# Kernel tuning notes

Hardware: AMD Instinct MI355X
Metric: run time of the kernel (lower is better)

The kernel has to match this reference:

```python
import jax, jax.numpy as jnp
import numpy as np

B = 32768
W = 7            # window_size (fixed: classifier head outputs 7*2 -> view(B, 7, 2))
F = 80           # per-frame feature size
WF = W * F       # window_feature_size = 560
EH = 512         # encoder_hidden_size
EO = 512         # encoder_output_size
H = 512          # core_hidden_size
NUM_STEPS = 7
EPS = 1e-5

def _linear(x, w, b):
    return x @ w.T + b

def _bn(x, g, bt, m, v):
    # BatchNorm1d in eval mode (running stats)
    return (x - m) * g / jnp.sqrt(v + EPS) + bt

def _ln(x, g, b):
    mu = x.mean(-1, keepdims=True)
    var = x.var(-1, keepdims=True)
    return (x - mu) / jnp.sqrt(var + EPS) * g + b

def setup_inputs():
    key = jax.random.key(0)
    ks = iter(jax.random.split(key, 40))
    def rn(shape, s=0.05):
        return jax.random.normal(next(ks), shape, dtype=jnp.float32) * s
    def rv(shape):
        return jax.random.uniform(next(ks), shape, dtype=jnp.float32) + 0.5
    return {
        'features': jax.random.normal(next(ks), (B, W, F), dtype=jnp.float32),
        'dec_w': rn((W, H)), 'dec_b': rn((W,)),
        'dec_bn_g': rv((W,)), 'dec_bn_b': rn((W,)), 'dec_bn_m': rn((W,)), 'dec_bn_v': rv((W,)),
        'ea1_w': rn((EH, W)), 'ea1_b': rn((EH,)),
        'ea1_bn_g': rv((EH,)), 'ea1_bn_b': rn((EH,)), 'ea1_bn_m': rn((EH,)), 'ea1_bn_v': rv((EH,)),
        'ea2_w': rn((EO, EH)), 'ea2_b': rn((EO,)),
        'ea2_bn_g': rv((EO,)), 'ea2_bn_b': rn((EO,)), 'ea2_bn_m': rn((EO,)), 'ea2_bn_v': rv((EO,)),
        'ei1_w': rn((EH, WF)), 'ei1_b': rn((EH,)),
        'ei1_bn_g': rv((EH,)), 'ei1_bn_b': rn((EH,)), 'ei1_bn_m': rn((EH,)), 'ei1_bn_v': rv((EH,)),
        'ei2_w': rn((EO, EH)), 'ei2_b': rn((EO,)),
        'ei2_bn_g': rv((EO,)), 'ei2_bn_b': rn((EO,)), 'ei2_bn_m': rn((EO,)), 'ei2_bn_v': rv((EO,)),
        'w_ih': rn((4 * H, EO)), 'w_hh': rn((4 * H, H)), 'b_ih': rn((4 * H,)), 'b_hh': rn((4 * H,)),
        'ln_g': rv((H,)), 'ln_b': rn((H,)),
        'cls_w': rn((2 * W, H)), 'cls_b': rn((2 * W,)),
    }

def _forward(features, dec_w, dec_b, dec_bn_g, dec_bn_b, dec_bn_m, dec_bn_v,
             ea1_w, ea1_b, ea1_bn_g, ea1_bn_b, ea1_bn_m, ea1_bn_v,
             ea2_w, ea2_b, ea2_bn_g, ea2_bn_b, ea2_bn_m, ea2_bn_v,
             ei1_w, ei1_b, ei1_bn_g, ei1_bn_b, ei1_bn_m, ei1_bn_v,
             ei2_w, ei2_b, ei2_bn_g, ei2_bn_b, ei2_bn_m, ei2_bn_v,
             w_ih, w_hh, b_ih, b_hh, ln_g, ln_b, cls_w, cls_b):
    Bsz = features.shape[0]

    def encoder(att):
        # attention branch: Linear -> BN -> ReLU -> Linear -> BN
        a = jax.nn.relu(_bn(_linear(att, ea1_w, ea1_b), ea1_bn_g, ea1_bn_b, ea1_bn_m, ea1_bn_v))
        a = _bn(_linear(a, ea2_w, ea2_b), ea2_bn_g, ea2_bn_b, ea2_bn_m, ea2_bn_v)
        # attended-input branch on flattened (features * att)
        ai = (features * att[:, :, None]).reshape(Bsz, WF)
        x = jax.nn.relu(_bn(_linear(ai, ei1_w, ei1_b), ei1_bn_g, ei1_bn_b, ei1_bn_m, ei1_bn_v))
        x = _bn(_linear(x, ei2_w, ei2_b), ei2_bn_g, ei2_bn_b, ei2_bn_m, ei2_bn_v)
        return jax.nn.relu(a + x)

    def lstm_step(x, h, c):
        gates = x @ w_ih.T + b_ih + h @ w_hh.T + b_hh  # [B, 4H], torch gate order i,f,g,o
        i, f, g, o = jnp.split(gates, 4, axis=-1)
        c = jax.nn.sigmoid(f) * c + jax.nn.sigmoid(i) * jnp.tanh(g)
        h = jax.nn.sigmoid(o) * jnp.tanh(c)
        return h, c

    # initial pass: uniform attention, zero LSTM state (state=None -> no LN)
    att0 = jnp.full((Bsz, W), 1.0 / W, dtype=features.dtype)
    h, c = lstm_step(encoder(att0), jnp.zeros((Bsz, H), features.dtype), jnp.zeros((Bsz, H), features.dtype))

    def body(carry, _):
        h, c = carry
        # decoder: Linear -> BN -> smooth softmax
        logits = _bn(_linear(h, dec_w, dec_b), dec_bn_g, dec_bn_b, dec_bn_m, dec_bn_v)
        s = jax.nn.sigmoid(logits)
        att = s / s.sum(-1, keepdims=True)
        agg = encoder(att)
        hn, cn = lstm_step(agg, _ln(h, ln_g, ln_b), _ln(c, ln_g, ln_b))
        return (hn, cn), None

    (h, c), _ = jax.lax.scan(body, (h, c), None, length=NUM_STEPS)
    out = _linear(h, cls_w, cls_b).reshape(Bsz, W, 2)
    return jax.nn.log_softmax(out, axis=2)

def reference(features, dec_w, dec_b, dec_bn_g, dec_bn_b, dec_bn_m, dec_bn_v,
              ea1_w, ea1_b, ea1_bn_g, ea1_bn_b, ea1_bn_m, ea1_bn_v,
              ea2_w, ea2_b, ea2_bn_g, ea2_bn_b, ea2_bn_m, ea2_bn_v,
              ei1_w, ei1_b, ei1_bn_g, ei1_bn_b, ei1_bn_m, ei1_bn_v,
              ei2_w, ei2_b, ei2_bn_g, ei2_bn_b, ei2_bn_m, ei2_bn_v,
              w_ih, w_hh, b_ih, b_hh, ln_g, ln_b, cls_w, cls_b):
    return _forward(features, dec_w, dec_b, dec_bn_g, dec_bn_b, dec_bn_m, dec_bn_v,
                    ea1_w, ea1_b, ea1_bn_g, ea1_bn_b, ea1_bn_m, ea1_bn_v,
                    ea2_w, ea2_b, ea2_bn_g, ea2_bn_b, ea2_bn_m, ea2_bn_v,
                    ei1_w, ei1_b, ei1_bn_g, ei1_bn_b, ei1_bn_m, ei1_bn_v,
                    ei2_w, ei2_b, ei2_bn_g, ei2_bn_b, ei2_bn_m, ei2_bn_v,
                    w_ih, w_hh, b_ih, b_hh, ln_g, ln_b, cls_w, cls_b)
```

## Files before the change

### kernel.cpp

```cpp
#include <hip/hip_runtime.h>
#include <cstdint>
#include <cstddef>

#define BSZ 32768
#define WN 7
#define WF 560
#define K1P 576
#define EPS 1e-5f

typedef __attribute__((ext_vector_type(8))) short bf16x8;
typedef __attribute__((ext_vector_type(4))) float f32x4;

__device__ __forceinline__ float b2f(short s) {
  union { float f; unsigned u; } x; x.u = ((unsigned)(unsigned short)s) << 16; return x.f;
}
__device__ __forceinline__ short f2b(float f) {
  union { float f; unsigned u; } x; x.f = f;
  unsigned r = x.u + 0x7fffu + ((x.u >> 16) & 1u);
  return (short)(r >> 16);
}
__device__ __forceinline__ float sigf(float x) { return 1.0f / (1.0f + __expf(-x)); }
__device__ __forceinline__ float ftanh(float x) {
  float t = __expf(-2.0f * fabsf(x));
  float r = (1.0f - t) / (1.0f + t);
  return copysignf(r, x);
}

__device__ __forceinline__ void async_copy16(const short* g, short* l) {
  __builtin_amdgcn_global_load_lds((const __attribute__((address_space(1))) unsigned*)g,
                                   (__attribute__((address_space(3))) unsigned*)l, 16, 0, 0);
}


__global__ void fold_small_k(const float* __restrict__ dec_w, const float* __restrict__ dec_b,
                             const float* __restrict__ dec_g, const float* __restrict__ dec_bt,
                             const float* __restrict__ dec_m, const float* __restrict__ dec_v,
                             const float* __restrict__ ea1_w, const float* __restrict__ ea1_b,
                             const float* __restrict__ ea1_g, const float* __restrict__ ea1_bt,
                             const float* __restrict__ ea1_m, const float* __restrict__ ea1_v,
                             float* __restrict__ decwf, float* __restrict__ decb8,
                             float* __restrict__ ea1f)
{
  int t = blockIdx.x * 256 + threadIdx.x;
  if (t < 7 * 512) {
    int w = t >> 9;
    float s = dec_g[w] * rsqrtf(dec_v[w] + EPS);
    decwf[t] = dec_w[t] * s;
  }
  if (t < 8) {
    if (t < 7) {
      float s = dec_g[t] * rsqrtf(dec_v[t] + EPS);
      decb8[t] = (dec_b[t] - dec_m[t]) * s + dec_bt[t];
    } else decb8[t] = 0.0f;
  }
  if (t < 512) {
    float s = ea1_g[t] * rsqrtf(ea1_v[t] + EPS);
    #pragma unroll
    for (int w = 0; w < 7; ++w) ea1f[t * 8 + w] = ea1_w[t * 7 + w] * s;
    ea1f[t * 8 + 7] = (ea1_b[t] - ea1_m[t]) * s + ea1_bt[t];
  }
}

__global__ void fold_ei1_k(const float* __restrict__ w, const float* __restrict__ b,
                           const float* __restrict__ g, const float* __restrict__ bt,
                           const float* __restrict__ m, const float* __restrict__ v,
                           short* __restrict__ ei1f, float* __restrict__ bias1)
{
  int idx = blockIdx.x * 256 + threadIdx.x;
  int n = idx / K1P, k = idx % K1P;
  float s = g[n] * rsqrtf(v[n] + EPS);
  ei1f[idx] = (k < WF) ? f2b(w[n * WF + k] * s) : (short)0;
  if (k == 0) bias1[n] = (b[n] - m[n]) * s + bt[n];
}

__global__ void fold_w2_k(const float* __restrict__ wi, const float* __restrict__ bi,
                          const float* __restrict__ gi, const float* __restrict__ bti,
                          const float* __restrict__ mi, const float* __restrict__ vi,
                          const float* __restrict__ wa, const float* __restrict__ ba,
                          const float* __restrict__ ga, const float* __restrict__ bta,
                          const float* __restrict__ ma, const float* __restrict__ va,
                          short* __restrict__ W2, float* __restrict__ bias2)
{
  int idx = blockIdx.x * 256 + threadIdx.x;
  int n = idx >> 10, k = idx & 1023;
  float si = gi[n] * rsqrtf(vi[n] + EPS);
  float sa = ga[n] * rsqrtf(va[n] + EPS);
  float val = (k < 512) ? wi[n * 512 + k] * si : wa[n * 512 + (k - 512)] * sa;
  W2[idx] = f2b(val);
  if (k == 0)
    bias2[n] = (bi[n] - mi[n]) * si + bti[n] + (ba[n] - ma[n]) * sa + bta[n];
}

__global__ void fold_wg_k(const float* __restrict__ w_ih, const float* __restrict__ w_hh,
                          const float* __restrict__ b_ih, const float* __restrict__ b_hh,
                          short* __restrict__ Wg, float* __restrict__ biasg)
{
  int idx = blockIdx.x * 256 + threadIdx.x;
  int c = idx >> 10, k = idx & 1023;
  int g = (c >> 4) & 3;
  int u = (c >> 6) * 16 + (c & 15);
  int r = g * 512 + u;
  float val = (k < 512) ? w_ih[r * 512 + k] : w_hh[r * 512 + (k - 512)];
  Wg[idx] = f2b(val);
  if (k == 0) biasg[c] = b_ih[r] + b_hh[r];
}

__global__ __launch_bounds__(512)
void attln_k(const float* __restrict__ hbuf, const float* __restrict__ cbuf,
             const float* __restrict__ decwf, const float* __restrict__ decb8,
             const float* __restrict__ ea1f,
             const float* __restrict__ ln_g, const float* __restrict__ ln_b,
             const float* __restrict__ feat,
             short* __restrict__ ghA, short* __restrict__ c_ln,
             short* __restrict__ xa, short* __restrict__ ai, int init)
{
  const int lane = threadIdx.x & 63;
  const int b = blockIdx.x * 8 + (threadIdx.x >> 6);
  float av[WN];
  if (init) {
    const float c7 = 1.0f / 7.0f;
    #pragma unroll
    for (int w = 0; w < WN; ++w) av[w] = c7;
    int4 z = make_int4(0, 0, 0, 0);
    *(int4*)&ghA[b * 1024 + 512 + lane * 8] = z;
    *(int4*)&c_ln[b * 512 + lane * 8] = z;
  } else {
    float hl[8];
    const float* hp = hbuf + (size_t)b * 512 + lane * 8;
    *(float4*)&hl[0] = *(const float4*)hp;
    *(float4*)&hl[4] = *(const float4*)(hp + 4);
    float s = 0.f, s2 = 0.f;
    #pragma unroll
    for (int e = 0; e < 8; ++e) { s += hl[e]; s2 += hl[e] * hl[e]; }
    float p[WN];
    #pragma unroll
    for (int w = 0; w < WN; ++w) {
      const float* dw = decwf + w * 512 + lane * 8;
      float4 w0 = *(const float4*)dw, w1 = *(const float4*)(dw + 4);
      p[w] = hl[0] * w0.x + hl[1] * w0.y + hl[2] * w0.z + hl[3] * w0.w
           + hl[4] * w1.x + hl[5] * w1.y + hl[6] * w1.z + hl[7] * w1.w;
    }
    #pragma unroll
    for (int o = 32; o > 0; o >>= 1) {
      s  += __shfl_xor(s, o);
      s2 += __shfl_xor(s2, o);
      #pragma unroll
      for (int w = 0; w < WN; ++w) p[w] += __shfl_xor(p[w], o);
    }
    float mu = s * (1.0f / 512.0f);
    float var = s2 * (1.0f / 512.0f) - mu * mu;
    float rstd = rsqrtf(var + EPS);
    float ssum = 0.f;
    #pragma unroll
    for (int w = 0; w < WN; ++w) { float sg = sigf(p[w] + decb8[w]); av[w] = sg; ssum += sg; }
    float inv = 1.0f / ssum;
    #pragma unroll
    for (int w = 0; w < WN; ++w) av[w] *= inv;
    short o8[8];
    #pragma unroll
    for (int e = 0; e < 8; ++e) {
      int i = lane * 8 + e;
      o8[e] = f2b((hl[e] - mu) * rstd * ln_g[i] + ln_b[i]);
    }
    *(int4*)&ghA[b * 1024 + 512 + lane * 8] = *(int4*)o8;
    float cl[8];
    const float* cp = cbuf + (size_t)b * 512 + lane * 8;
    *(float4*)&cl[0] = *(const float4*)cp;
    *(float4*)&cl[4] = *(const float4*)(cp + 4);
    float cs = 0.f, cs2 = 0.f;
    #pragma unroll
    for (int e = 0; e < 8; ++e) { cs += cl[e]; cs2 += cl[e] * cl[e]; }
    #pragma unroll
    for (int o = 32; o > 0; o >>= 1) {
      cs  += __shfl_xor(cs, o);
      cs2 += __shfl_xor(cs2, o);
    }
    float cmu = cs * (1.0f / 512.0f);
    float cvar = cs2 * (1.0f / 512.0f) - cmu * cmu;
    float crstd = rsqrtf(cvar + EPS);
    #pragma unroll
    for (int e = 0; e < 8; ++e) {
      int i = lane * 8 + e;
      o8[e] = f2b((cl[e] - cmu) * crstd * ln_g[i] + ln_b[i]);
    }
    *(int4*)&c_ln[b * 512 + lane * 8] = *(int4*)o8;
  }
  short a8[8];
  #pragma unroll
  for (int e = 0; e < 8; ++e) {
    int n = lane * 8 + e;
    const float* wr = ea1f + n * 8;
    float4 w0 = *(const float4*)wr, w1 = *(const float4*)(wr + 4);
    float v = w1.w
            + av[0] * w0.x + av[1] * w0.y + av[2] * w0.z + av[3] * w0.w
            + av[4] * w1.x + av[5] * w1.y + av[6] * w1.z;
    a8[e] = f2b(fmaxf(v, 0.0f));
  }
  *(int4*)&xa[b * 1024 + 512 + lane * 8] = *(int4*)a8;
  const float* fr = feat + (size_t)b * WF;
  short* air = ai + (size_t)b * K1P;
  #pragma unroll
  for (int rr = 0; rr < 2; ++rr) {
    int c8 = lane + rr * 64;
    if (c8 < 72) {
      int k = c8 * 8;
      short s8[8];
      if (k < WF) {
        int window = c8 / 10;
        float a = av[0];
        #pragma unroll
        for (int w = 1; w < WN; ++w) a = (window == w) ? av[w] : a;
        float4 f0 = *(const float4*)(fr + k);
        float4 f1 = *(const float4*)(fr + k + 4);
        s8[0] = f2b(f0.x * a); s8[1] = f2b(f0.y * a); s8[2] = f2b(f0.z * a); s8[3] = f2b(f0.w * a);
        s8[4] = f2b(f1.x * a); s8[5] = f2b(f1.y * a); s8[6] = f2b(f1.z * a); s8[7] = f2b(f1.w * a);
      } else {
        #pragma unroll
        for (int e = 0; e < 8; ++e) s8[e] = 0;
      }
      *(int4*)&air[k] = *(int4*)s8;
    }
  }
}

#define STAGE128(SRC, LD, K0, S) do {                                          \
    _Pragma("unroll")                                                          \
    for (int r_ = 0; r_ < 4; ++r_) {                                           \
      int idx_ = r_ * 256 + t;                                                 \
      int row_ = idx_ >> 3, dcol_ = (idx_ & 7) * 8;                            \
      int scol_ = dcol_ ^ ((row_ & 7) << 3);                                   \
      async_copy16(SRC + (size_t)row_ * (LD) + (K0) + scol_, &S[idx_ * 8]);    \
    }                                                                          \
  } while (0)

#define READ_FRAG(S, ROW, KS) \
  (*(const bf16x8*)&S[(ROW) * 64 + (((KS)) ^ (((ROW) & 7) << 3))])

__global__ __launch_bounds__(256)
void gemm_bt_k(const short* __restrict__ A, int lda,
               const short* __restrict__ Wt, int K,
               const float* __restrict__ bias,
               short* __restrict__ C, int ldc)
{
  const int bswz = blockIdx.x;
  const int xcd = bswz & 7, slot = bswz >> 3;
  const int m0 = (xcd + 8 * (slot >> 2)) * 128;
  const int n0 = (slot & 3) * 128;
  __shared__ short sA[128 * 64];
  __shared__ short sB[128 * 64];
  const int t = threadIdx.x;
  const int wv = t >> 6, lane = t & 63;
  const int wm = (wv & 1) * 64, wn = (wv >> 1) * 64;
  const int lr = lane & 15, lk = (lane >> 4) * 8;

  f32x4 acc[4][4] = {};
  const short* Ab = A + (size_t)m0 * lda;
  const short* Wb = Wt + (size_t)n0 * K;

  for (int k0 = 0; k0 < K; k0 += 64) {
    STAGE128(Ab, lda, k0, sA);
    STAGE128(Wb, K, k0, sB);
    __syncthreads();
    #pragma unroll
    for (int ks = 0; ks < 64; ks += 32) {
      bf16x8 af[4], bfr[4];
      #pragma unroll
      for (int i = 0; i < 4; ++i) af[i]  = READ_FRAG(sA, wm + i * 16 + lr, ks + lk);
      #pragma unroll
      for (int j = 0; j < 4; ++j) bfr[j] = READ_FRAG(sB, wn + j * 16 + lr, ks + lk);
      #pragma unroll
      for (int i = 0; i < 4; ++i)
        #pragma unroll
        for (int j = 0; j < 4; ++j)
          acc[i][j] = __builtin_amdgcn_mfma_f32_16x16x32_bf16(af[i], bfr[j], acc[i][j], 0, 0, 0);
    }
    __syncthreads();
  }
  #pragma unroll
  for (int j = 0; j < 4; ++j) {
    int col = n0 + wn + j * 16 + lr;
    float bs = bias[col];
    #pragma unroll
    for (int i = 0; i < 4; ++i) {
      int rbase = m0 + wm + i * 16 + (lane >> 4) * 4;
      #pragma unroll
      for (int e = 0; e < 4; ++e) {
        float v = acc[i][j][e] + bs;
        C[(size_t)(rbase + e) * ldc + col] = f2b(fmaxf(v, 0.0f));
      }
    }
  }
}


#define G_STAGE(g) do {                                                              \
    short* dA_ = &sA[((g) % 3) * 16384];                                             \
    short* dB_ = &sB[((g) % 3) * 8192];                                              \
    _Pragma("unroll")                                                                \
    for (int q_ = 0; q_ < 4; ++q_) {                                                 \
      int idx_ = q_ * 512 + t;                                                       \
      int row_ = idx_ >> 3, ds_ = idx_ & 7;                                          \
      int sc_ = (ds_ ^ (row_ & 7)) * 8;                                              \
      async_copy16(A + (size_t)(m0 + row_) * 1024 + (g) * 64 + sc_, dA_ + idx_ * 8); \
    }                                                                                \
    _Pragma("unroll")                                                                \
    for (int q_ = 0; q_ < 2; ++q_) {                                                 \
      int idx_ = q_ * 512 + t;                                                       \
      int row_ = idx_ >> 3, ds_ = idx_ & 7;                                          \
      int sc_ = (ds_ ^ (row_ & 7)) * 8;                                              \
      async_copy16(Wg + (size_t)(n0 + row_) * 1024 + (g) * 64 + sc_, dB_ + idx_ * 8);\
    }                                                                                \
  } while (0)

#define G_COMPUTE(g) do {                                                            \
    const short* bA_ = &sA[((g) % 3) * 16384];                                       \
    const short* bB_ = &sB[((g) % 3) * 8192];                                        \
    bf16x8 af_[4][2], bf_[4][2];                                                     \
    _Pragma("unroll")                                                                \
    for (int mf_ = 0; mf_ < 4; ++mf_) {                                              \
      int row_ = wm * 64 + mf_ * 16 + lr;                                            \
      _Pragma("unroll")                                                              \
      for (int ks_ = 0; ks_ < 2; ++ks_)                                              \
        af_[mf_][ks_] = *(const bf16x8*)&bA_[row_ * 64 + (((ks_ * 4 + hi) ^ (row_ & 7)) * 8)]; \
    }                                                                                \
    _Pragma("unroll")                                                                \
    for (int nf_ = 0; nf_ < 4; ++nf_) {                                              \
      int row_ = wn * 64 + nf_ * 16 + lr;                                            \
      _Pragma("unroll")                                                              \
      for (int ks_ = 0; ks_ < 2; ++ks_)                                              \
        bf_[nf_][ks_] = *(const bf16x8*)&bB_[row_ * 64 + (((ks_ * 4 + hi) ^ (row_ & 7)) * 8)]; \
    }                                                                                \
    __builtin_amdgcn_s_setprio(1);                                                   \
    _Pragma("unroll")                                                                \
    for (int mf_ = 0; mf_ < 4; ++mf_)                                                \
      _Pragma("unroll")                                                              \
      for (int nf_ = 0; nf_ < 4; ++nf_) {                                            \
        acc[mf_][nf_] = __builtin_amdgcn_mfma_f32_16x16x32_bf16(af_[mf_][0], bf_[nf_][0], acc[mf_][nf_], 0, 0, 0); \
        acc[mf_][nf_] = __builtin_amdgcn_mfma_f32_16x16x32_bf16(af_[mf_][1], bf_[nf_][1], acc[mf_][nf_], 0, 0, 0); \
      }                                                                              \
    __builtin_amdgcn_s_setprio(0);                                                   \
  } while (0)

__global__ __launch_bounds__(512, 2)
void gates_k(const short* __restrict__ A,
             const short* __restrict__ Wg,
             const float* __restrict__ biasg,
             const short* __restrict__ c_ln,
             float* __restrict__ hbuf, float* __restrict__ cbuf)
{
  __shared__ short sA[3 * 256 * 64];
  __shared__ short sB[3 * 128 * 64];
  const int bswz = blockIdx.x;
  const int xcd = bswz & 7, slot = bswz >> 3;
  const int m0 = (xcd + 8 * (slot >> 4)) * 256;
  const int n0 = (slot & 15) * 128;
  const int t = threadIdx.x;
  const int wid = t >> 6, lane = t & 63;
  const int wm = wid >> 1, wn = wid & 1;
  const int lr = lane & 15, hi = lane >> 4;

  f32x4 acc[4][4] = {};

  G_STAGE(0);
  G_STAGE(1);
  asm volatile("s_waitcnt vmcnt(6)" ::: "memory");
  __builtin_amdgcn_s_barrier();

  #pragma unroll
  for (int g = 0; g < 16; ++g) {
    if (g + 2 < 16) G_STAGE(g + 2);
    G_COMPUTE(g);
    if (g < 14)
      asm volatile("s_waitcnt vmcnt(6) lgkmcnt(0)" ::: "memory");
    else if (g == 14)
      asm volatile("s_waitcnt vmcnt(0) lgkmcnt(0)" ::: "memory");
    if (g < 15) __builtin_amdgcn_s_barrier();
  }

  const int u = ((n0 + wn * 64) >> 6) * 16 + lr;
  const float bi_ = biasg[n0 + wn * 64 + 0 * 16 + lr];
  const float bf2 = biasg[n0 + wn * 64 + 1 * 16 + lr];
  const float bg_ = biasg[n0 + wn * 64 + 2 * 16 + lr];
  const float bo_ = biasg[n0 + wn * 64 + 3 * 16 + lr];
  #pragma unroll
  for (int mf = 0; mf < 4; ++mf) {
    int rbase = m0 + wm * 64 + mf * 16 + hi * 4;
    #pragma unroll
    for (int e = 0; e < 4; ++e) {
      int row = rbase + e;
      float iv = sigf(acc[mf][0][e] + bi_);
      float fv = sigf(acc[mf][1][e] + bf2);
      float gv = ftanh(acc[mf][2][e] + bg_);
      float ov = sigf(acc[mf][3][e] + bo_);
      float cold = b2f(c_ln[(size_t)row * 512 + u]);
      float cc = fv * cold + iv * gv;
      hbuf[(size_t)row * 512 + u] = ov * ftanh(cc);
      cbuf[(size_t)row * 512 + u] = cc;
    }
  }
}

__global__ __launch_bounds__(512)
void cls_k(const float* __restrict__ hbuf, const float* __restrict__ cw,
           const float* __restrict__ cb, float* __restrict__ out)
{
  const int lane = threadIdx.x & 63;
  const int b = blockIdx.x * 8 + (threadIdx.x >> 6);
  float hl[8];
  const float* hp = hbuf + (size_t)b * 512 + lane * 8;
  *(float4*)&hl[0] = *(const float4*)hp;
  *(float4*)&hl[4] = *(const float4*)(hp + 4);
  float p[14];
  #pragma unroll
  for (int tcol = 0; tcol < 14; ++tcol) {
    const float* wr = cw + tcol * 512 + lane * 8;
    float4 w0 = *(const float4*)wr, w1 = *(const float4*)(wr + 4);
    p[tcol] = hl[0] * w0.x + hl[1] * w0.y + hl[2] * w0.z + hl[3] * w0.w
            + hl[4] * w1.x + hl[5] * w1.y + hl[6] * w1.z + hl[7] * w1.w;
  }
  #pragma unroll
  for (int o = 32; o > 0; o >>= 1)
    #pragma unroll
    for (int tcol = 0; tcol < 14; ++tcol) p[tcol] += __shfl_xor(p[tcol], o);
  if (lane < 14) {
    float z = cb[lane];
    #pragma unroll
    for (int tcol = 0; tcol < 14; ++tcol) if (lane == tcol) z += p[tcol];
    float zp = __shfl_xor(z, 1);
    float m = fmaxf(z, zp);
    float l = m + __logf(__expf(z - m) + __expf(zp - m));
    out[(size_t)b * 14 + lane] = z - l;
  }
}


extern "C" void kernel_launch(void* const* d_in, const int* in_sizes, int n_in,
                              void* d_out, int out_size, void* d_ws, size_t ws_size,
                              hipStream_t stream)
{
  const float* features = (const float*)d_in[0];
  const float* dec_w    = (const float*)d_in[1];
  const float* dec_b    = (const float*)d_in[2];
  const float* dec_bn_g = (const float*)d_in[3];
  const float* dec_bn_b = (const float*)d_in[4];
  const float* dec_bn_m = (const float*)d_in[5];
  const float* dec_bn_v = (const float*)d_in[6];
  const float* ea1_w    = (const float*)d_in[7];
  const float* ea1_b    = (const float*)d_in[8];
  const float* ea1_bn_g = (const float*)d_in[9];
  const float* ea1_bn_b = (const float*)d_in[10];
  const float* ea1_bn_m = (const float*)d_in[11];
  const float* ea1_bn_v = (const float*)d_in[12];
  const float* ea2_w    = (const float*)d_in[13];
  const float* ea2_b    = (const float*)d_in[14];
  const float* ea2_bn_g = (const float*)d_in[15];
  const float* ea2_bn_b = (const float*)d_in[16];
  const float* ea2_bn_m = (const float*)d_in[17];
  const float* ea2_bn_v = (const float*)d_in[18];
  const float* ei1_w    = (const float*)d_in[19];
  const float* ei1_b    = (const float*)d_in[20];
  const float* ei1_bn_g = (const float*)d_in[21];
  const float* ei1_bn_b = (const float*)d_in[22];
  const float* ei1_bn_m = (const float*)d_in[23];
  const float* ei1_bn_v = (const float*)d_in[24];
  const float* ei2_w    = (const float*)d_in[25];
  const float* ei2_b    = (const float*)d_in[26];
  const float* ei2_bn_g = (const float*)d_in[27];
  const float* ei2_bn_b = (const float*)d_in[28];
  const float* ei2_bn_m = (const float*)d_in[29];
  const float* ei2_bn_v = (const float*)d_in[30];
  const float* w_ih     = (const float*)d_in[31];
  const float* w_hh     = (const float*)d_in[32];
  const float* b_ih     = (const float*)d_in[33];
  const float* b_hh     = (const float*)d_in[34];
  const float* ln_g     = (const float*)d_in[35];
  const float* ln_b     = (const float*)d_in[36];
  const float* cls_w    = (const float*)d_in[37];
  const float* cls_b    = (const float*)d_in[38];
  (void)in_sizes; (void)n_in; (void)out_size;

  int chunk = BSZ;
  while (chunk > 2048 && (size_t)chunk * 10368 + (16u << 20) > ws_size) chunk >>= 1;

  char* ws = (char*)d_ws;
  size_t off = 0;
  auto carve = [&](size_t bytes) -> void* {
    void* p = ws + off;
    off += (bytes + 255) & ~(size_t)255;
    return p;
  };
  short* ei1f  = (short*)carve((size_t)512 * K1P * 2);
  float* bias1 = (float*)carve(512 * 4);
  short* W2    = (short*)carve((size_t)512 * 1024 * 2);
  float* bias2 = (float*)carve(512 * 4);
  short* Wg    = (short*)carve((size_t)2048 * 1024 * 2);
  float* biasg = (float*)carve(2048 * 4);
  float* decwf = (float*)carve(7 * 512 * 4);
  float* decb8 = (float*)carve(8 * 4);
  float* ea1f  = (float*)carve(512 * 8 * 4);
  float* hbuf  = (float*)carve((size_t)chunk * 512 * 4);
  float* cbuf  = (float*)carve((size_t)chunk * 512 * 4);
  short* ghA   = (short*)carve((size_t)chunk * 1024 * 2);
  short* xa    = (short*)carve((size_t)chunk * 1024 * 2);
  short* clnb  = (short*)carve((size_t)chunk * 512 * 2);
  short* ai    = (short*)carve((size_t)chunk * K1P * 2);

  fold_small_k<<<16, 256, 0, stream>>>(dec_w, dec_b, dec_bn_g, dec_bn_b, dec_bn_m, dec_bn_v,
                                       ea1_w, ea1_b, ea1_bn_g, ea1_bn_b, ea1_bn_m, ea1_bn_v,
                                       decwf, decb8, ea1f);
  fold_ei1_k<<<(512 * K1P) / 256, 256, 0, stream>>>(ei1_w, ei1_b, ei1_bn_g, ei1_bn_b,
                                                    ei1_bn_m, ei1_bn_v, ei1f, bias1);
  fold_w2_k<<<(512 * 1024) / 256, 256, 0, stream>>>(ei2_w, ei2_b, ei2_bn_g, ei2_bn_b, ei2_bn_m, ei2_bn_v,
                                                    ea2_w, ea2_b, ea2_bn_g, ea2_bn_b, ea2_bn_m, ea2_bn_v,
                                                    W2, bias2);
  fold_wg_k<<<(2048 * 1024) / 256, 256, 0, stream>>>(w_ih, w_hh, b_ih, b_hh, Wg, biasg);

  for (int base = 0; base < BSZ; base += chunk) {
    const float* featc = features + (size_t)base * WF;
    float* outc = (float*)d_out + (size_t)base * 14;
    for (int s = 0; s < 8; ++s) {
      attln_k<<<chunk / 8, 512, 0, stream>>>(hbuf, cbuf, decwf, decb8, ea1f, ln_g, ln_b,
                                             featc, ghA, clnb, xa, ai, (s == 0) ? 1 : 0);
      gemm_bt_k<<<(chunk / 128) * 4, 256, 0, stream>>>(ai, K1P, ei1f, K1P, bias1, xa, 1024);
      gemm_bt_k<<<(chunk / 128) * 4, 256, 0, stream>>>(xa, 1024, W2, 1024, bias2, ghA, 1024);
      gates_k<<<(chunk / 256) * 16, 512, 0, stream>>>(ghA, Wg, biasg, clnb, hbuf, cbuf);
    }
    cls_k<<<chunk / 8, 512, 0, stream>>>(hbuf, cls_w, cls_b, outc);
  }
}
```

Before: 2.825 ms.

## Enlarge gates GEMM tile to 256x256 with double buffering

The LSTM gates kernel's block tile grows from 256x128 to 256x256, so each wave now holds 4x8 accumulators and each k-step loads fragments per k-slice. The shared-memory pipeline goes from triple to double buffering, and the XCD-aware block swizzle is replaced by a plain 2D grid. The aim is more operand reuse per byte loaded and half as many blocks re-reading A. The cost is higher register pressure (128 accumulator floats per lane) that may break the 2-blocks-per-CU occupancy, a shallower prefetch depth with full vmcnt(0) waits, and a loss of L2 locality from the dropped swizzle.

```diff
diff --git a/kernel.cpp b/kernel.cpp
--- a/kernel.cpp
+++ b/kernel.cpp
@@ -293,9 +293,9 @@
 }
 
 
-#define G_STAGE(g) do {                                                              \
-    short* dA_ = &sA[((g) % 3) * 16384];                                             \
-    short* dB_ = &sB[((g) % 3) * 8192];                                              \
+#define GS_STAGE(g) do {                                                             \
+    short* dA_ = &sA[((g) & 1) * 16384];                                             \
+    short* dB_ = &sB[((g) & 1) * 16384];                                             \
     _Pragma("unroll")                                                                \
     for (int q_ = 0; q_ < 4; ++q_) {                                                 \
       int idx_ = q_ * 512 + t;                                                       \
@@ -304,7 +304,7 @@
       async_copy16(A + (size_t)(m0 + row_) * 1024 + (g) * 64 + sc_, dA_ + idx_ * 8); \
     }                                                                                \
     _Pragma("unroll")                                                                \
-    for (int q_ = 0; q_ < 2; ++q_) {                                                 \
+    for (int q_ = 0; q_ < 4; ++q_) {                                                 \
       int idx_ = q_ * 512 + t;                                                       \
       int row_ = idx_ >> 3, ds_ = idx_ & 7;                                          \
       int sc_ = (ds_ ^ (row_ & 7)) * 8;                                              \
@@ -312,33 +312,30 @@
     }                                                                                \
   } while (0)
 
-#define G_COMPUTE(g) do {                                                            \
-    const short* bA_ = &sA[((g) % 3) * 16384];                                       \
-    const short* bB_ = &sB[((g) % 3) * 8192];                                        \
-    bf16x8 af_[4][2], bf_[4][2];                                                     \
+#define GS_COMPUTE(g) do {                                                           \
+    const short* bA_ = &sA[((g) & 1) * 16384];                                       \
+    const short* bB_ = &sB[((g) & 1) * 16384];                                       \
     _Pragma("unroll")                                                                \
-    for (int mf_ = 0; mf_ < 4; ++mf_) {                                              \
-      int row_ = wm * 64 + mf_ * 16 + lr;                                            \
+    for (int ks_ = 0; ks_ < 2; ++ks_) {                                              \
+      bf16x8 af_[4], bf_[8];                                                         \
       _Pragma("unroll")                                                              \
-      for (int ks_ = 0; ks_ < 2; ++ks_)                                              \
-        af_[mf_][ks_] = *(const bf16x8*)&bA_[row_ * 64 + (((ks_ * 4 + hi) ^ (row_ & 7)) * 8)]; \
+      for (int mf_ = 0; mf_ < 4; ++mf_) {                                            \
+        int row_ = wm * 64 + mf_ * 16 + lr;                                          \
+        af_[mf_] = *(const bf16x8*)&bA_[row_ * 64 + (((ks_ * 4 + hi) ^ (row_ & 7)) * 8)]; \
+      }                                                                              \
+      _Pragma("unroll")                                                              \
+      for (int nf_ = 0; nf_ < 8; ++nf_) {                                            \
+        int row_ = wn * 128 + nf_ * 16 + lr;                                         \
+        bf_[nf_] = *(const bf16x8*)&bB_[row_ * 64 + (((ks_ * 4 + hi) ^ (row_ & 7)) * 8)]; \
+      }                                                                              \
+      __builtin_amdgcn_s_setprio(1);                                                 \
+      _Pragma("unroll")                                                              \
+      for (int mf_ = 0; mf_ < 4; ++mf_)                                              \
+        _Pragma("unroll")                                                            \
+        for (int nf_ = 0; nf_ < 8; ++nf_)                                            \
+          acc[mf_][nf_] = __builtin_amdgcn_mfma_f32_16x16x32_bf16(af_[mf_], bf_[nf_], acc[mf_][nf_], 0, 0, 0); \
+      __builtin_amdgcn_s_setprio(0);                                                 \
     }                                                                                \
-    _Pragma("unroll")                                                                \
-    for (int nf_ = 0; nf_ < 4; ++nf_) {                                              \
-      int row_ = wn * 64 + nf_ * 16 + lr;                                            \
-      _Pragma("unroll")                                                              \
-      for (int ks_ = 0; ks_ < 2; ++ks_)                                              \
-        bf_[nf_][ks_] = *(const bf16x8*)&bB_[row_ * 64 + (((ks_ * 4 + hi) ^ (row_ & 7)) * 8)]; \
-    }                                                                                \
-    __builtin_amdgcn_s_setprio(1);                                                   \
-    _Pragma("unroll")                                                                \
-    for (int mf_ = 0; mf_ < 4; ++mf_)                                                \
-      _Pragma("unroll")                                                              \
-      for (int nf_ = 0; nf_ < 4; ++nf_) {                                            \
-        acc[mf_][nf_] = __builtin_amdgcn_mfma_f32_16x16x32_bf16(af_[mf_][0], bf_[nf_][0], acc[mf_][nf_], 0, 0, 0); \
-        acc[mf_][nf_] = __builtin_amdgcn_mfma_f32_16x16x32_bf16(af_[mf_][1], bf_[nf_][1], acc[mf_][nf_], 0, 0, 0); \
-      }                                                                              \
-    __builtin_amdgcn_s_setprio(0);                                                   \
   } while (0)
 
 __global__ __launch_bounds__(512, 2)
@@ -348,54 +345,54 @@
              const short* __restrict__ c_ln,
              float* __restrict__ hbuf, float* __restrict__ cbuf)
 {
-  __shared__ short sA[3 * 256 * 64];
-  __shared__ short sB[3 * 128 * 64];
-  const int bswz = blockIdx.x;
-  const int xcd = bswz & 7, slot = bswz >> 3;
-  const int m0 = (xcd + 8 * (slot >> 4)) * 256;
-  const int n0 = (slot & 15) * 128;
+  __shared__ short sA[2 * 256 * 64];
+  __shared__ short sB[2 * 256 * 64];
+  const int m0 = blockIdx.x * 256;
+  const int n0 = blockIdx.y * 256;
   const int t = threadIdx.x;
   const int wid = t >> 6, lane = t & 63;
   const int wm = wid >> 1, wn = wid & 1;
   const int lr = lane & 15, hi = lane >> 4;
 
-  f32x4 acc[4][4] = {};
-
-  G_STAGE(0);
-  G_STAGE(1);
-  asm volatile("s_waitcnt vmcnt(6)" ::: "memory");
+  f32x4 acc[4][8] = {};
+
+  GS_STAGE(0);
+  asm volatile("s_waitcnt vmcnt(0)" ::: "memory");
   __builtin_amdgcn_s_barrier();
 
   #pragma unroll
   for (int g = 0; g < 16; ++g) {
-    if (g + 2 < 16) G_STAGE(g + 2);
-    G_COMPUTE(g);
-    if (g < 14)
-      asm volatile("s_waitcnt vmcnt(6) lgkmcnt(0)" ::: "memory");
-    else if (g == 14)
+    if (g + 1 < 16) GS_STAGE(g + 1);
+    GS_COMPUTE(g);
+    if (g + 1 < 16) {
       asm volatile("s_waitcnt vmcnt(0) lgkmcnt(0)" ::: "memory");
-    if (g < 15) __builtin_amdgcn_s_barrier();
-  }
-
-  const int u = ((n0 + wn * 64) >> 6) * 16 + lr;
-  const float bi_ = biasg[n0 + wn * 64 + 0 * 16 + lr];
-  const float bf2 = biasg[n0 + wn * 64 + 1 * 16 + lr];
-  const float bg_ = biasg[n0 + wn * 64 + 2 * 16 + lr];
-  const float bo_ = biasg[n0 + wn * 64 + 3 * 16 + lr];
-  #pragma unroll
-  for (int mf = 0; mf < 4; ++mf) {
-    int rbase = m0 + wm * 64 + mf * 16 + hi * 4;
-    #pragma unroll
-    for (int e = 0; e < 4; ++e) {
-      int row = rbase + e;
-      float iv = sigf(acc[mf][0][e] + bi_);
-      float fv = sigf(acc[mf][1][e] + bf2);
-      float gv = ftanh(acc[mf][2][e] + bg_);
-      float ov = sigf(acc[mf][3][e] + bo_);
-      float cold = b2f(c_ln[(size_t)row * 512 + u]);
-      float cc = fv * cold + iv * gv;
-      hbuf[(size_t)row * 512 + u] = ov * ftanh(cc);
-      cbuf[(size_t)row * 512 + u] = cc;
+      __builtin_amdgcn_s_barrier();
+    }
+  }
+
+  #pragma unroll
+  for (int grp = 0; grp < 2; ++grp) {
+    const int cb = n0 + wn * 128 + grp * 64;
+    const int u = ((cb >> 6)) * 16 + lr;
+    const float bi_ = biasg[cb + 0 * 16 + lr];
+    const float bf2 = biasg[cb + 1 * 16 + lr];
+    const float bg_ = biasg[cb + 2 * 16 + lr];
+    const float bo_ = biasg[cb + 3 * 16 + lr];
+    #pragma unroll
+    for (int mf = 0; mf < 4; ++mf) {
+      int rbase = m0 + wm * 64 + mf * 16 + hi * 4;
+      #pragma unroll
+      for (int e = 0; e < 4; ++e) {
+        int row = rbase + e;
+        float iv = sigf(acc[mf][grp * 4 + 0][e] + bi_);
+        float fv = sigf(acc[mf][grp * 4 + 1][e] + bf2);
+        float gv = ftanh(acc[mf][grp * 4 + 2][e] + bg_);
+        float ov = sigf(acc[mf][grp * 4 + 3][e] + bo_);
+        float cold = b2f(c_ln[(size_t)row * 512 + u]);
+        float cc = fv * cold + iv * gv;
+        hbuf[(size_t)row * 512 + u] = ov * ftanh(cc);
+        cbuf[(size_t)row * 512 + u] = cc;
+      }
     }
   }
 }
@@ -523,7 +520,7 @@
                                              featc, ghA, clnb, xa, ai, (s == 0) ? 1 : 0);
       gemm_bt_k<<<(chunk / 128) * 4, 256, 0, stream>>>(ai, K1P, ei1f, K1P, bias1, xa, 1024);
       gemm_bt_k<<<(chunk / 128) * 4, 256, 0, stream>>>(xa, 1024, W2, 1024, bias2, ghA, 1024);
-      gates_k<<<(chunk / 256) * 16, 512, 0, stream>>>(ghA, Wg, biasg, clnb, hbuf, cbuf);
+      gates_k<<<dim3(chunk / 256, 8), 512, 0, stream>>>(ghA, Wg, biasg, clnb, hbuf, cbuf);
     }
     cls_k<<<chunk / 8, 512, 0, stream>>>(hbuf, cls_w, cls_b, outc);
   }
```

Measured after the change: 2.765 ms. -2.1%, faster.
